# Kernel optimization log

Hardware: AMD Instinct MI355X
Metric: run time of the kernel (lower is better)

## Reference

```python
import jax, jax.numpy as jnp
import numpy as np

LN_EPS = 1e-5
L2_EPS = 1e-12  # torch F.normalize eps


def _layernorm(h, g, b):
    mu = jnp.mean(h, axis=-1, keepdims=True)
    var = jnp.var(h, axis=-1, keepdims=True)
    return (h - mu) * jax.lax.rsqrt(var + LN_EPS) * g + b


def _l2norm(h):
    n = jnp.linalg.norm(h, axis=-1, keepdims=True)
    return h / jnp.maximum(n, L2_EPS)


def _temperature(epoch, total_epochs):
    warmup = total_epochs * 0.1
    if epoch < warmup:
        return 2.0
    progress = (epoch - warmup) / (total_epochs - warmup)
    return max(0.7, 2.0 - 1.3 * progress)


def setup_inputs() -> dict:
    key = jax.random.key(0)
    ks = jax.random.split(key, 4)
    B, T, D, P, C = 8, 4096, 1024, 512, 64
    x = jax.random.normal(ks[0], (B, T, D), dtype=jnp.float32)
    w1 = jax.random.normal(ks[1], (D, C), dtype=jnp.float32) * 0.02
    b1 = jnp.zeros((C,), jnp.float32)
    ln1_g = jnp.ones((C,), jnp.float32)
    ln1_b = jnp.zeros((C,), jnp.float32)
    patterns = jax.random.normal(ks[2], (P, C), dtype=jnp.float32)
    patterns = _l2norm(patterns)  # init is row-orthonormalized in torch via SVD; unit rows suffice
    w2 = jax.random.normal(ks[3], (C, D), dtype=jnp.float32) * 0.02
    b2 = jnp.zeros((D,), jnp.float32)
    ln2_g = jnp.ones((D,), jnp.float32)
    ln2_b = jnp.zeros((D,), jnp.float32)
    return {"x": x, "w1": w1, "b1": b1, "ln1_g": ln1_g, "ln1_b": ln1_b,
            "patterns": patterns, "w2": w2, "b2": b2, "ln2_g": ln2_g, "ln2_b": ln2_b,
            "epoch": 0, "total_epochs": 100}


def reference(x, w1, b1, ln1_g, ln1_b, patterns, w2, b2, ln2_g, ln2_b, epoch, total_epochs):
    n_patterns = patterns.shape[0]
    # bottleneck projection + LayerNorm: [B,T,D] -> [B,T,C]
    Q = _layernorm(jnp.einsum('btd,dc->btc', x, w1) + b1, ln1_g, ln1_b)
    Q_norm = _l2norm(Q)
    K_norm = _l2norm(patterns)  # [P,C]
    temp = _temperature(epoch, total_epochs)
    logits = jnp.einsum('btc,pc->btp', Q_norm, K_norm) / temp  # [B,T,P]
    hard_indices = jnp.argmax(logits, axis=-1)  # [B,T]
    assignments = jax.nn.one_hot(hard_indices, n_patterns, dtype=jnp.float32)  # eval: hard
    pattern_emb_low = jnp.einsum('btp,pc->btc', assignments, patterns)
    pattern_emb = _layernorm(jnp.einsum('btc,cd->btd', pattern_emb_low, w2) + b2, ln2_g, ln2_b)
    return (pattern_emb, assignments, logits, hard_indices, Q)
```

## Files before the change

### kernel.cpp

```cpp
#include <hip/hip_runtime.h>

#define O_PE 0
#define O_AS 33554432
#define O_LG 50331648
#define O_HI 67108864
#define O_Q  67141632

typedef float vf4 __attribute__((ext_vector_type(4)));

__device__ __forceinline__ void nts4(float* p, float4 v) {
  vf4 t; t.x = v.x; t.y = v.y; t.z = v.z; t.w = v.w;
  __builtin_nontemporal_store(t, (vf4*)p);
}
__device__ __forceinline__ float4 ntl4(const float* p) {
  vf4 t = __builtin_nontemporal_load((const vf4*)p);
  float4 r; r.x = t.x; r.y = t.y; r.z = t.z; r.w = t.w;
  return r;
}

__global__ void k0_pre(const float* __restrict__ patterns, const float* __restrict__ w2,
                       const float* __restrict__ b2, const float* __restrict__ ln2g,
                       const float* __restrict__ ln2b, const int* __restrict__ epoch,
                       const int* __restrict__ total_epochs,
                       float* __restrict__ invt, float* __restrict__ knT,
                       float* __restrict__ peb) {
  const int b = blockIdx.x, t = threadIdx.x;
  __shared__ float pat[64];
  __shared__ float red[8];

  if (b == 0 && t == 0) {
    float ep = (float)epoch[0], te = (float)total_epochs[0];
    float warm = te * 0.1f;
    float temp;
    if (ep < warm) temp = 2.0f;
    else {
      float prog = (ep - warm) / (te - warm);
      temp = fmaxf(0.7f, 2.0f - 1.3f * prog);
    }
    invt[0] = 1.0f / temp;
  }

  if (t < 64) pat[t] = patterns[b * 64 + t];
  __syncthreads();

  if (t < 64) {
    float v = pat[t];
    float s = v * v;
    #pragma unroll
    for (int m = 1; m < 64; m <<= 1) s += __shfl_xor(s, m);
    float scale = 1.0f / fmaxf(sqrtf(s), 1e-12f);
    knT[(size_t)t * 512 + b] = v * scale;
  }

  const int d0 = t * 4;
  float4 acc = *(const float4*)&b2[d0];
  #pragma unroll 8
  for (int k = 0; k < 64; ++k) {
    float pk = pat[k];
    float4 w = *(const float4*)&w2[(size_t)k * 1024 + d0];
    acc.x = fmaf(pk, w.x, acc.x);
    acc.y = fmaf(pk, w.y, acc.y);
    acc.z = fmaf(pk, w.z, acc.z);
    acc.w = fmaf(pk, w.w, acc.w);
  }
  float s1 = acc.x + acc.y + acc.z + acc.w;
  float s2 = acc.x*acc.x + acc.y*acc.y + acc.z*acc.z + acc.w*acc.w;
  #pragma unroll
  for (int m = 1; m < 64; m <<= 1) { s1 += __shfl_xor(s1, m); s2 += __shfl_xor(s2, m); }
  const int wid = t >> 6;
  if ((t & 63) == 0) { red[wid] = s1; red[wid + 4] = s2; }
  __syncthreads();
  s1 = red[0] + red[1] + red[2] + red[3];
  s2 = red[4] + red[5] + red[6] + red[7];
  float mu = s1 * (1.0f / 1024.0f);
  float var = s2 * (1.0f / 1024.0f) - mu * mu;
  float rstd = rsqrtf(var + 1e-5f);
  float4 g  = *(const float4*)&ln2g[d0];
  float4 bb = *(const float4*)&ln2b[d0];
  float4 o;
  o.x = (acc.x - mu) * rstd * g.x + bb.x;
  o.y = (acc.y - mu) * rstd * g.y + bb.y;
  o.z = (acc.z - mu) * rstd * g.z + bb.z;
  o.w = (acc.w - mu) * rstd * g.w + bb.w;
  *(float4*)&peb[(size_t)b * 1024 + d0] = o;
}

__global__ __launch_bounds__(256, 2) void k_fused(
    const float* __restrict__ x, const float* __restrict__ w1,
    const float* __restrict__ b1, const float* __restrict__ ln1g,
    const float* __restrict__ ln1b, const float* __restrict__ knT,
    const float* __restrict__ invtp, const float* __restrict__ peb,
    float* __restrict__ outPe, float* __restrict__ outAs,
    float* __restrict__ outLg, float* __restrict__ outHi,
    float* __restrict__ outQ) {
  __shared__ float smem[17408];
  const int tid = threadIdx.x;
  const int rowbase = blockIdx.x * 64;

  const int g  = tid >> 6;
  const int t  = tid & 63;
  const int rt = t >> 3, ct = t & 7;
  const int r0 = rt * 8, c0 = ct * 8;
  const int kbase = g * 256;

  float* xsT = smem;
  float* w1s = smem + 8704;

  float acc[8][8];
  #pragma unroll
  for (int i = 0; i < 8; ++i)
    #pragma unroll
    for (int j = 0; j < 8; ++j) acc[i][j] = 0.f;

  const float* xp = x + (size_t)(rowbase + (t >> 3)) * 1024 + kbase + (t & 7) * 4;
  const int wkr = t >> 4;
  const int wc4 = (t & 15) * 4;

  for (int kt = 0; kt < 8; ++kt) {
    const int kb = kt * 32;
    float4 xv[8], wv[8];
    #pragma unroll
    for (int p = 0; p < 8; ++p)
      xv[p] = ntl4(xp + (size_t)p * 8192 + kb);
    const float* wp = w1 + (size_t)(kbase + kb + wkr) * 64 + wc4;
    #pragma unroll
    for (int p = 0; p < 8; ++p)
      wv[p] = *(const float4*)(wp + (size_t)p * 256);
    __syncthreads();
    {
      const int kc4 = (t & 7) * 4;
      const int sw = 8 * ((kc4 >> 3) & 3);
      #pragma unroll
      for (int p = 0; p < 8; ++p) {
        const int row = ((t >> 3) + 8 * p) ^ sw;
        xsT[g*2176 + (kc4+0)*68 + row] = xv[p].x;
        xsT[g*2176 + (kc4+1)*68 + row] = xv[p].y;
        xsT[g*2176 + (kc4+2)*68 + row] = xv[p].z;
        xsT[g*2176 + (kc4+3)*68 + row] = xv[p].w;
      }
    }
    #pragma unroll
    for (int p = 0; p < 8; ++p)
      *(float4*)&w1s[g*2176 + (wkr + 4*p)*68 + wc4] = wv[p];
    __syncthreads();
    #pragma unroll 4
    for (int kk = 0; kk < 32; ++kk) {
      const int rb = r0 ^ (8 * ((kk >> 3) & 3));
      float4 a0 = *(float4*)&xsT[g*2176 + kk*68 + rb];
      float4 a1 = *(float4*)&xsT[g*2176 + kk*68 + rb + 4];
      float4 b0 = *(float4*)&w1s[g*2176 + kk*68 + c0];
      float4 b1v = *(float4*)&w1s[g*2176 + kk*68 + c0 + 4];
      float av[8] = {a0.x, a0.y, a0.z, a0.w, a1.x, a1.y, a1.z, a1.w};
      float bv[8] = {b0.x, b0.y, b0.z, b0.w, b1v.x, b1v.y, b1v.z, b1v.w};
      #pragma unroll
      for (int i = 0; i < 8; ++i)
        #pragma unroll
        for (int j = 0; j < 8; ++j)
          acc[i][j] = fmaf(av[i], bv[j], acc[i][j]);
    }
  }

  __syncthreads();
  if (g > 0) {
    float* hc = smem + (g - 1) * 4096;
    #pragma unroll
    for (int i = 0; i < 8; ++i) {
      float4 v0, v1;
      v0.x = acc[i][0]; v0.y = acc[i][1]; v0.z = acc[i][2]; v0.w = acc[i][3];
      v1.x = acc[i][4]; v1.y = acc[i][5]; v1.z = acc[i][6]; v1.w = acc[i][7];
      *(float4*)&hc[(r0+i)*64 + c0]     = v0;
      *(float4*)&hc[(r0+i)*64 + c0 + 4] = v1;
    }
  }
  __syncthreads();
  float* qns = smem + 12288;
  if (g == 0) {
    float bb[8], gg[8], ee[8];
    {
      float4 t0 = *(const float4*)&b1[c0];
      float4 t1 = *(const float4*)&b1[c0 + 4];
      float4 t2 = *(const float4*)&ln1g[c0];
      float4 t3 = *(const float4*)&ln1g[c0 + 4];
      float4 t4 = *(const float4*)&ln1b[c0];
      float4 t5 = *(const float4*)&ln1b[c0 + 4];
      bb[0]=t0.x; bb[1]=t0.y; bb[2]=t0.z; bb[3]=t0.w; bb[4]=t1.x; bb[5]=t1.y; bb[6]=t1.z; bb[7]=t1.w;
      gg[0]=t2.x; gg[1]=t2.y; gg[2]=t2.z; gg[3]=t2.w; gg[4]=t3.x; gg[5]=t3.y; gg[6]=t3.z; gg[7]=t3.w;
      ee[0]=t4.x; ee[1]=t4.y; ee[2]=t4.z; ee[3]=t4.w; ee[4]=t5.x; ee[5]=t5.y; ee[6]=t5.z; ee[7]=t5.w;
    }
    #pragma unroll
    for (int i = 0; i < 8; ++i) {
      const int row = r0 + i;
      float h[8];
      #pragma unroll
      for (int j = 0; j < 8; ++j) h[j] = acc[i][j] + bb[j];
      #pragma unroll
      for (int gg2 = 0; gg2 < 3; ++gg2) {
        float4 p0 = *(float4*)&smem[gg2*4096 + row*64 + c0];
        float4 p1 = *(float4*)&smem[gg2*4096 + row*64 + c0 + 4];
        h[0] += p0.x; h[1] += p0.y; h[2] += p0.z; h[3] += p0.w;
        h[4] += p1.x; h[5] += p1.y; h[6] += p1.z; h[7] += p1.w;
      }
      float s1 = 0.f, s2 = 0.f;
      #pragma unroll
      for (int j = 0; j < 8; ++j) { s1 += h[j]; s2 += h[j]*h[j]; }
      #pragma unroll
      for (int m = 1; m < 8; m <<= 1) { s1 += __shfl_xor(s1, m); s2 += __shfl_xor(s2, m); }
      const float mu   = s1 * 0.015625f;
      const float var  = s2 * 0.015625f - mu * mu;
      const float rstd = rsqrtf(var + 1e-5f);
      float q[8]; float t2s = 0.f;
      #pragma unroll
      for (int j = 0; j < 8; ++j) { q[j] = (h[j] - mu) * rstd * gg[j] + ee[j]; t2s += q[j]*q[j]; }
      #pragma unroll
      for (int m = 1; m < 8; m <<= 1) t2s += __shfl_xor(t2s, m);
      const float scl = 1.0f / fmaxf(sqrtf(t2s), 1e-12f);
      float4 qa, qc;
      qa.x = q[0]; qa.y = q[1]; qa.z = q[2]; qa.w = q[3];
      qc.x = q[4]; qc.y = q[5]; qc.z = q[6]; qc.w = q[7];
      nts4(&outQ[(size_t)(rowbase + row) * 64 + c0], qa);
      nts4(&outQ[(size_t)(rowbase + row) * 64 + c0 + 4], qc);
      #pragma unroll
      for (int j = 0; j < 8; ++j) qns[row*68 + c0 + j] = q[j] * scl;
    }
  }
  __syncthreads();

  const float invt = invtp[0];
  const int lane = tid & 63;
  const int w    = tid >> 6;
  const int brt  = lane & 3;
  const int pt16 = lane >> 2;
  const int pbase = w * 128 + pt16 * 8;

  float* avm = smem;
  int*   avi = (int*)(smem + 256);
  int*   sidx = (int*)(smem + 512);

  float a2[16][8];
  #pragma unroll
  for (int i = 0; i < 16; ++i)
    #pragma unroll
    for (int j = 0; j < 8; ++j) a2[i][j] = 0.f;

  for (int cb = 0; cb < 16; ++cb) {
    float kv[4][8];
    #pragma unroll
    for (int dc = 0; dc < 4; ++dc) {
      float4 k0 = *(const float4*)&knT[(size_t)(cb*4+dc)*512 + pbase];
      float4 k1 = *(const float4*)&knT[(size_t)(cb*4+dc)*512 + pbase + 4];
      kv[dc][0]=k0.x; kv[dc][1]=k0.y; kv[dc][2]=k0.z; kv[dc][3]=k0.w;
      kv[dc][4]=k1.x; kv[dc][5]=k1.y; kv[dc][6]=k1.z; kv[dc][7]=k1.w;
    }
    #pragma unroll
    for (int i = 0; i < 16; ++i) {
      float4 qv = *(float4*)&qns[(brt + 4*i)*68 + cb*4];
      float qq[4] = {qv.x, qv.y, qv.z, qv.w};
      #pragma unroll
      for (int dc = 0; dc < 4; ++dc)
        #pragma unroll
        for (int j = 0; j < 8; ++j)
          a2[i][j] = fmaf(qq[dc], kv[dc][j], a2[i][j]);
    }
  }

  #pragma unroll
  for (int i = 0; i < 16; ++i) {
    const int row = brt + 4*i;
    const size_t grow = (size_t)(rowbase + row);
    float v[8];
    float bm = -3.0e38f; int bi = 0;
    #pragma unroll
    for (int j = 0; j < 8; ++j) {
      v[j] = a2[i][j] * invt;
      if (v[j] > bm) { bm = v[j]; bi = pbase + j; }
    }
    float4 o0, o1;
    o0.x = v[0]; o0.y = v[1]; o0.z = v[2]; o0.w = v[3];
    o1.x = v[4]; o1.y = v[5]; o1.z = v[6]; o1.w = v[7];
    nts4(&outLg[grow * 512 + pbase], o0);
    nts4(&outLg[grow * 512 + pbase + 4], o1);
    #pragma unroll
    for (int m = 4; m < 64; m <<= 1) {
      float ov = __shfl_xor(bm, m);
      int   oi = __shfl_xor(bi, m);
      if (ov > bm || (ov == bm && oi < bi)) { bm = ov; bi = oi; }
    }
    if (pt16 == 0) { avm[w*64 + row] = bm; avi[w*64 + row] = bi; }
  }
  __syncthreads();

  if (tid < 64) {
    float bm = avm[tid]; int bi = avi[tid];
    #pragma unroll
    for (int w2 = 1; w2 < 4; ++w2) {
      float m = avm[w2*64 + tid];
      int   i = avi[w2*64 + tid];
      if (m > bm) { bm = m; bi = i; }
    }
    sidx[tid] = bi;
    __builtin_nontemporal_store((float)bi, &outHi[rowbase + tid]);
  }
  __syncthreads();

  #pragma unroll
  for (int p = 0; p < 32; ++p) {
    const int id = tid + p * 256;
    const int r = id >> 7, c4 = (id & 127) * 4;
    const int b = sidx[r];
    float4 z; z.x = 0.f; z.y = 0.f; z.z = 0.f; z.w = 0.f;
    if (b >= c4 && b < c4 + 4) ((float*)&z)[b - c4] = 1.0f;
    nts4(&outAs[(size_t)(rowbase + r) * 512 + c4], z);
  }

  #pragma unroll 4
  for (int p = 0; p < 64; ++p) {
    const int id = tid + p * 256;
    const int r = id >> 8, c4 = id & 255;
    float4 pv = *(const float4*)&peb[((size_t)sidx[r] * 256 + c4) * 4];
    nts4(&outPe[((size_t)(rowbase + r) * 256 + c4) * 4], pv);
  }
}

extern "C" void kernel_launch(void* const* d_in, const int* in_sizes, int n_in,
                              void* d_out, int out_size, void* d_ws, size_t ws_size,
                              hipStream_t stream) {
  (void)in_sizes; (void)n_in; (void)out_size; (void)ws_size;
  const float* x        = (const float*)d_in[0];
  const float* w1       = (const float*)d_in[1];
  const float* b1       = (const float*)d_in[2];
  const float* ln1g     = (const float*)d_in[3];
  const float* ln1b     = (const float*)d_in[4];
  const float* patterns = (const float*)d_in[5];
  const float* w2       = (const float*)d_in[6];
  const float* b2       = (const float*)d_in[7];
  const float* ln2g     = (const float*)d_in[8];
  const float* ln2b     = (const float*)d_in[9];
  const int*   epoch    = (const int*)d_in[10];
  const int*   total    = (const int*)d_in[11];

  float* out = (float*)d_out;
  float* outPe = out + O_PE;
  float* outAs = out + O_AS;
  float* outLg = out + O_LG;
  float* outHi = out + O_HI;
  float* outQ  = out + O_Q;

  float* wsf  = (float*)d_ws;
  float* invt = wsf;
  float* knT  = wsf + 64;
  float* peb  = (float*)((char*)d_ws + 131328);

  hipLaunchKernelGGL(k0_pre, dim3(512), dim3(256), 0, stream,
                     patterns, w2, b2, ln2g, ln2b, epoch, total, invt, knT, peb);
  hipLaunchKernelGGL(k_fused, dim3(512), dim3(256), 0, stream,
                     x, w1, b1, ln1g, ln1b, knT, invt, peb,
                     outPe, outAs, outLg, outHi, outQ);
}
```

Baseline: 156.2 us.

## Double block size to 512 threads with 8-way split-K and tree reduction

Launches the fused kernel with 512 threads per block instead of 256. The first GEMM's K dimension is now split across 8 wavefront groups of 128 instead of 4 of 256, and partial sums are combined with a shared-memory tree reduction. The logits stage and the output writes are also redistributed so each thread handles half as many rows. The aim is more waves in flight for latency hiding on this memory-bound kernel, at the cost of extra barriers and reduction steps and possibly tighter register limits from the launch bounds.

```diff
diff --git a/kernel.cpp b/kernel.cpp
--- a/kernel.cpp
+++ b/kernel.cpp
@@ -85,7 +85,7 @@
   *(float4*)&peb[(size_t)b * 1024 + d0] = o;
 }
 
-__global__ __launch_bounds__(256, 2) void k_fused(
+__global__ __launch_bounds__(512, 4) void k_fused(
     const float* __restrict__ x, const float* __restrict__ w1,
     const float* __restrict__ b1, const float* __restrict__ ln1g,
     const float* __restrict__ ln1b, const float* __restrict__ knT,
@@ -101,10 +101,10 @@
   const int t  = tid & 63;
   const int rt = t >> 3, ct = t & 7;
   const int r0 = rt * 8, c0 = ct * 8;
-  const int kbase = g * 256;
-
-  float* xsT = smem;
-  float* w1s = smem + 8704;
+  const int kbase = g * 128;
+
+  float* xsT = smem + g * 1088;
+  float* w1s = smem + 8704 + g * 1088;
 
   float acc[8][8];
   #pragma unroll
@@ -112,44 +112,43 @@
     #pragma unroll
     for (int j = 0; j < 8; ++j) acc[i][j] = 0.f;
 
-  const float* xp = x + (size_t)(rowbase + (t >> 3)) * 1024 + kbase + (t & 7) * 4;
+  const int srow = t >> 2;
+  const int skc4 = (t & 3) * 4;
+  const int ssw  = 8 * ((skc4 >> 3) & 1);
+  const float* xp = x + (size_t)(rowbase + srow) * 1024 + kbase + skc4;
   const int wkr = t >> 4;
   const int wc4 = (t & 15) * 4;
+  const float* wp0 = w1 + (size_t)(kbase + wkr) * 64 + wc4;
 
   for (int kt = 0; kt < 8; ++kt) {
-    const int kb = kt * 32;
-    float4 xv[8], wv[8];
-    #pragma unroll
-    for (int p = 0; p < 8; ++p)
-      xv[p] = ntl4(xp + (size_t)p * 8192 + kb);
-    const float* wp = w1 + (size_t)(kbase + kb + wkr) * 64 + wc4;
-    #pragma unroll
-    for (int p = 0; p < 8; ++p)
-      wv[p] = *(const float4*)(wp + (size_t)p * 256);
+    const int kb = kt * 16;
+    float4 xv[4], wv[4];
+    #pragma unroll
+    for (int p = 0; p < 4; ++p)
+      xv[p] = ntl4(xp + (size_t)p * 16384 + kb);
+    #pragma unroll
+    for (int p = 0; p < 4; ++p)
+      wv[p] = *(const float4*)(wp0 + (size_t)(kb + 4 * p) * 64);
     __syncthreads();
-    {
-      const int kc4 = (t & 7) * 4;
-      const int sw = 8 * ((kc4 >> 3) & 3);
-      #pragma unroll
-      for (int p = 0; p < 8; ++p) {
-        const int row = ((t >> 3) + 8 * p) ^ sw;
-        xsT[g*2176 + (kc4+0)*68 + row] = xv[p].x;
-        xsT[g*2176 + (kc4+1)*68 + row] = xv[p].y;
-        xsT[g*2176 + (kc4+2)*68 + row] = xv[p].z;
-        xsT[g*2176 + (kc4+3)*68 + row] = xv[p].w;
-      }
-    }
-    #pragma unroll
-    for (int p = 0; p < 8; ++p)
-      *(float4*)&w1s[g*2176 + (wkr + 4*p)*68 + wc4] = wv[p];
+    #pragma unroll
+    for (int p = 0; p < 4; ++p) {
+      const int row = (srow + 16 * p) ^ ssw;
+      xsT[(skc4+0)*68 + row] = xv[p].x;
+      xsT[(skc4+1)*68 + row] = xv[p].y;
+      xsT[(skc4+2)*68 + row] = xv[p].z;
+      xsT[(skc4+3)*68 + row] = xv[p].w;
+    }
+    #pragma unroll
+    for (int p = 0; p < 4; ++p)
+      *(float4*)&w1s[(wkr + 4*p)*68 + wc4] = wv[p];
     __syncthreads();
     #pragma unroll 4
-    for (int kk = 0; kk < 32; ++kk) {
-      const int rb = r0 ^ (8 * ((kk >> 3) & 3));
-      float4 a0 = *(float4*)&xsT[g*2176 + kk*68 + rb];
-      float4 a1 = *(float4*)&xsT[g*2176 + kk*68 + rb + 4];
-      float4 b0 = *(float4*)&w1s[g*2176 + kk*68 + c0];
-      float4 b1v = *(float4*)&w1s[g*2176 + kk*68 + c0 + 4];
+    for (int kk = 0; kk < 16; ++kk) {
+      const int rb = r0 ^ (8 * ((kk >> 3) & 1));
+      float4 a0 = *(float4*)&xsT[kk*68 + rb];
+      float4 a1 = *(float4*)&xsT[kk*68 + rb + 4];
+      float4 b0 = *(float4*)&w1s[kk*68 + c0];
+      float4 b1v = *(float4*)&w1s[kk*68 + c0 + 4];
       float av[8] = {a0.x, a0.y, a0.z, a0.w, a1.x, a1.y, a1.z, a1.w};
       float bv[8] = {b0.x, b0.y, b0.z, b0.w, b1v.x, b1v.y, b1v.z, b1v.w};
       #pragma unroll
@@ -161,8 +160,8 @@
   }
 
   __syncthreads();
-  if (g > 0) {
-    float* hc = smem + (g - 1) * 4096;
+  if (g & 1) {
+    float* hc = smem + (g >> 1) * 4096;
     #pragma unroll
     for (int i = 0; i < 8; ++i) {
       float4 v0, v1;
@@ -173,7 +172,53 @@
     }
   }
   __syncthreads();
-  float* qns = smem + 12288;
+  if (!(g & 1)) {
+    float* hc = smem + (g >> 1) * 4096;
+    #pragma unroll
+    for (int i = 0; i < 8; ++i) {
+      float4 p0 = *(float4*)&hc[(r0+i)*64 + c0];
+      float4 p1 = *(float4*)&hc[(r0+i)*64 + c0 + 4];
+      acc[i][0] += p0.x; acc[i][1] += p0.y; acc[i][2] += p0.z; acc[i][3] += p0.w;
+      acc[i][4] += p1.x; acc[i][5] += p1.y; acc[i][6] += p1.z; acc[i][7] += p1.w;
+    }
+  }
+  __syncthreads();
+  if (g == 2 || g == 6) {
+    float* hc = smem + ((g - 2) >> 2) * 4096;
+    #pragma unroll
+    for (int i = 0; i < 8; ++i) {
+      float4 v0, v1;
+      v0.x = acc[i][0]; v0.y = acc[i][1]; v0.z = acc[i][2]; v0.w = acc[i][3];
+      v1.x = acc[i][4]; v1.y = acc[i][5]; v1.z = acc[i][6]; v1.w = acc[i][7];
+      *(float4*)&hc[(r0+i)*64 + c0]     = v0;
+      *(float4*)&hc[(r0+i)*64 + c0 + 4] = v1;
+    }
+  }
+  __syncthreads();
+  if (g == 0 || g == 4) {
+    float* hc = smem + (g >> 2) * 4096;
+    #pragma unroll
+    for (int i = 0; i < 8; ++i) {
+      float4 p0 = *(float4*)&hc[(r0+i)*64 + c0];
+      float4 p1 = *(float4*)&hc[(r0+i)*64 + c0 + 4];
+      acc[i][0] += p0.x; acc[i][1] += p0.y; acc[i][2] += p0.z; acc[i][3] += p0.w;
+      acc[i][4] += p1.x; acc[i][5] += p1.y; acc[i][6] += p1.z; acc[i][7] += p1.w;
+    }
+  }
+  __syncthreads();
+  if (g == 4) {
+    #pragma unroll
+    for (int i = 0; i < 8; ++i) {
+      float4 v0, v1;
+      v0.x = acc[i][0]; v0.y = acc[i][1]; v0.z = acc[i][2]; v0.w = acc[i][3];
+      v1.x = acc[i][4]; v1.y = acc[i][5]; v1.z = acc[i][6]; v1.w = acc[i][7];
+      *(float4*)&smem[(r0+i)*64 + c0]     = v0;
+      *(float4*)&smem[(r0+i)*64 + c0 + 4] = v1;
+    }
+  }
+  __syncthreads();
+
+  float* qns = smem + 8704;
   if (g == 0) {
     float bb[8], gg[8], ee[8];
     {
@@ -193,13 +238,10 @@
       float h[8];
       #pragma unroll
       for (int j = 0; j < 8; ++j) h[j] = acc[i][j] + bb[j];
-      #pragma unroll
-      for (int gg2 = 0; gg2 < 3; ++gg2) {
-        float4 p0 = *(float4*)&smem[gg2*4096 + row*64 + c0];
-        float4 p1 = *(float4*)&smem[gg2*4096 + row*64 + c0 + 4];
-        h[0] += p0.x; h[1] += p0.y; h[2] += p0.z; h[3] += p0.w;
-        h[4] += p1.x; h[5] += p1.y; h[6] += p1.z; h[7] += p1.w;
-      }
+      float4 p0 = *(float4*)&smem[row*64 + c0];
+      float4 p1 = *(float4*)&smem[row*64 + c0 + 4];
+      h[0] += p0.x; h[1] += p0.y; h[2] += p0.z; h[3] += p0.w;
+      h[4] += p1.x; h[5] += p1.y; h[6] += p1.z; h[7] += p1.w;
       float s1 = 0.f, s2 = 0.f;
       #pragma unroll
       for (int j = 0; j < 8; ++j) { s1 += h[j]; s2 += h[j]*h[j]; }
@@ -227,18 +269,18 @@
 
   const float invt = invtp[0];
   const int lane = tid & 63;
-  const int w    = tid >> 6;
-  const int brt  = lane & 3;
-  const int pt16 = lane >> 2;
-  const int pbase = w * 128 + pt16 * 8;
-
-  float* avm = smem;
-  int*   avi = (int*)(smem + 256);
-  int*   sidx = (int*)(smem + 512);
-
-  float a2[16][8];
+  const int w8   = tid >> 6;
+  const int pt8  = lane >> 3;
+  const int brt  = lane & 7;
+  const int pbase = w8 * 64 + pt8 * 8;
+
+  float* avm = smem + 13056;
+  int*   avi = (int*)(smem + 13568);
+  int*   sidx = (int*)(smem + 14080);
+
+  float a2[8][8];
   #pragma unroll
-  for (int i = 0; i < 16; ++i)
+  for (int i = 0; i < 8; ++i)
     #pragma unroll
     for (int j = 0; j < 8; ++j) a2[i][j] = 0.f;
 
@@ -252,8 +294,8 @@
       kv[dc][4]=k1.x; kv[dc][5]=k1.y; kv[dc][6]=k1.z; kv[dc][7]=k1.w;
     }
     #pragma unroll
-    for (int i = 0; i < 16; ++i) {
-      float4 qv = *(float4*)&qns[(brt + 4*i)*68 + cb*4];
+    for (int i = 0; i < 8; ++i) {
+      float4 qv = *(float4*)&qns[(brt + 8*i)*68 + cb*4];
       float qq[4] = {qv.x, qv.y, qv.z, qv.w};
       #pragma unroll
       for (int dc = 0; dc < 4; ++dc)
@@ -264,8 +306,8 @@
   }
 
   #pragma unroll
-  for (int i = 0; i < 16; ++i) {
-    const int row = brt + 4*i;
+  for (int i = 0; i < 8; ++i) {
+    const int row = brt + 8*i;
     const size_t grow = (size_t)(rowbase + row);
     float v[8];
     float bm = -3.0e38f; int bi = 0;
@@ -280,19 +322,19 @@
     nts4(&outLg[grow * 512 + pbase], o0);
     nts4(&outLg[grow * 512 + pbase + 4], o1);
     #pragma unroll
-    for (int m = 4; m < 64; m <<= 1) {
+    for (int m = 8; m < 64; m <<= 1) {
       float ov = __shfl_xor(bm, m);
       int   oi = __shfl_xor(bi, m);
       if (ov > bm || (ov == bm && oi < bi)) { bm = ov; bi = oi; }
     }
-    if (pt16 == 0) { avm[w*64 + row] = bm; avi[w*64 + row] = bi; }
+    if (pt8 == 0) { avm[w8*64 + row] = bm; avi[w8*64 + row] = bi; }
   }
   __syncthreads();
 
   if (tid < 64) {
     float bm = avm[tid]; int bi = avi[tid];
     #pragma unroll
-    for (int w2 = 1; w2 < 4; ++w2) {
+    for (int w2 = 1; w2 < 8; ++w2) {
       float m = avm[w2*64 + tid];
       int   i = avi[w2*64 + tid];
       if (m > bm) { bm = m; bi = i; }
@@ -303,8 +345,8 @@
   __syncthreads();
 
   #pragma unroll
-  for (int p = 0; p < 32; ++p) {
-    const int id = tid + p * 256;
+  for (int p = 0; p < 16; ++p) {
+    const int id = tid + p * 512;
     const int r = id >> 7, c4 = (id & 127) * 4;
     const int b = sidx[r];
     float4 z; z.x = 0.f; z.y = 0.f; z.z = 0.f; z.w = 0.f;
@@ -313,8 +355,8 @@
   }
 
   #pragma unroll 4
-  for (int p = 0; p < 64; ++p) {
-    const int id = tid + p * 256;
+  for (int p = 0; p < 32; ++p) {
+    const int id = tid + p * 512;
     const int r = id >> 8, c4 = id & 255;
     float4 pv = *(const float4*)&peb[((size_t)sidx[r] * 256 + c4) * 4];
     nts4(&outPe[((size_t)(rowbase + r) * 256 + c4) * 4], pv);
@@ -352,7 +394,7 @@
 
   hipLaunchKernelGGL(k0_pre, dim3(512), dim3(256), 0, stream,
                      patterns, w2, b2, ln2g, ln2b, epoch, total, invt, knT, peb);
-  hipLaunchKernelGGL(k_fused, dim3(512), dim3(256), 0, stream,
+  hipLaunchKernelGGL(k_fused, dim3(512), dim3(512), 0, stream,
                      x, w1, b1, ln1g, ln1b, knT, invt, peb,
                      outPe, outAs, outLg, outHi, outQ);
 }
```

Result: slower. 169.5 us (+8.5%).

## Halve rows per block and drop LDS staging for the projection GEMM

Applied to the files above, without the earlier changes.

Each block now handles 32 rows instead of 64, doubling the grid to 1024 blocks. The x·w1 projection reads x and w1 straight from global memory into registers instead of staging transposed tiles in shared memory, which removes per-tile barriers and cuts LDS use. The split-K partial sums are reduced as a tree in shared memory. The aim is more resident blocks and better latency hiding on this memory-bound kernel, at the cost of redundant w1 reads through cache and less reuse per thread.

```diff
diff --git a/kernel.cpp b/kernel.cpp
--- a/kernel.cpp
+++ b/kernel.cpp
@@ -93,113 +93,113 @@
     float* __restrict__ outPe, float* __restrict__ outAs,
     float* __restrict__ outLg, float* __restrict__ outHi,
     float* __restrict__ outQ) {
-  __shared__ float smem[17408];
+  __shared__ float smem[6560];
   const int tid = threadIdx.x;
-  const int rowbase = blockIdx.x * 64;
+  const int rowbase = blockIdx.x * 32;
 
   const int g  = tid >> 6;
   const int t  = tid & 63;
   const int rt = t >> 3, ct = t & 7;
-  const int r0 = rt * 8, c0 = ct * 8;
   const int kbase = g * 256;
 
-  float* xsT = smem;
-  float* w1s = smem + 8704;
-
-  float acc[8][8];
-  #pragma unroll
-  for (int i = 0; i < 8; ++i)
+  float acc[4][8];
+  #pragma unroll
+  for (int i = 0; i < 4; ++i)
     #pragma unroll
     for (int j = 0; j < 8; ++j) acc[i][j] = 0.f;
 
-  const float* xp = x + (size_t)(rowbase + (t >> 3)) * 1024 + kbase + (t & 7) * 4;
-  const int wkr = t >> 4;
-  const int wc4 = (t & 15) * 4;
-
-  for (int kt = 0; kt < 8; ++kt) {
-    const int kb = kt * 32;
-    float4 xv[8], wv[8];
-    #pragma unroll
-    for (int p = 0; p < 8; ++p)
-      xv[p] = ntl4(xp + (size_t)p * 8192 + kb);
-    const float* wp = w1 + (size_t)(kbase + kb + wkr) * 64 + wc4;
-    #pragma unroll
-    for (int p = 0; p < 8; ++p)
-      wv[p] = *(const float4*)(wp + (size_t)p * 256);
-    __syncthreads();
-    {
-      const int kc4 = (t & 7) * 4;
-      const int sw = 8 * ((kc4 >> 3) & 3);
-      #pragma unroll
-      for (int p = 0; p < 8; ++p) {
-        const int row = ((t >> 3) + 8 * p) ^ sw;
-        xsT[g*2176 + (kc4+0)*68 + row] = xv[p].x;
-        xsT[g*2176 + (kc4+1)*68 + row] = xv[p].y;
-        xsT[g*2176 + (kc4+2)*68 + row] = xv[p].z;
-        xsT[g*2176 + (kc4+3)*68 + row] = xv[p].w;
-      }
-    }
-    #pragma unroll
-    for (int p = 0; p < 8; ++p)
-      *(float4*)&w1s[g*2176 + (wkr + 4*p)*68 + wc4] = wv[p];
-    __syncthreads();
-    #pragma unroll 4
-    for (int kk = 0; kk < 32; ++kk) {
-      const int rb = r0 ^ (8 * ((kk >> 3) & 3));
-      float4 a0 = *(float4*)&xsT[g*2176 + kk*68 + rb];
-      float4 a1 = *(float4*)&xsT[g*2176 + kk*68 + rb + 4];
-      float4 b0 = *(float4*)&w1s[g*2176 + kk*68 + c0];
-      float4 b1v = *(float4*)&w1s[g*2176 + kk*68 + c0 + 4];
-      float av[8] = {a0.x, a0.y, a0.z, a0.w, a1.x, a1.y, a1.z, a1.w};
-      float bv[8] = {b0.x, b0.y, b0.z, b0.w, b1v.x, b1v.y, b1v.z, b1v.w};
-      #pragma unroll
-      for (int i = 0; i < 8; ++i)
-        #pragma unroll
-        for (int j = 0; j < 8; ++j)
-          acc[i][j] = fmaf(av[i], bv[j], acc[i][j]);
-    }
-  }
-
-  __syncthreads();
-  if (g > 0) {
-    float* hc = smem + (g - 1) * 4096;
-    #pragma unroll
-    for (int i = 0; i < 8; ++i) {
+  const float* xa = x + (size_t)(rowbase + rt) * 1024 + kbase;
+  const float* wb = w1 + (size_t)kbase * 64 + ct * 8;
+
+  #pragma unroll 2
+  for (int kk4 = 0; kk4 < 64; ++kk4) {
+    float4 av[4];
+    #pragma unroll
+    for (int i = 0; i < 4; ++i)
+      av[i] = ntl4(xa + (size_t)8192 * i + 4 * kk4);
+    const float* wk = wb + (size_t)(4 * kk4) * 64;
+#define ASTEP(DC, COMP)                                                     \
+    {                                                                       \
+      float4 b0 = *(const float4*)(wk + (size_t)DC * 64);                   \
+      float4 b1v = *(const float4*)(wk + (size_t)DC * 64 + 4);              \
+      _Pragma("unroll")                                                     \
+      for (int i = 0; i < 4; ++i) {                                         \
+        const float ai = av[i].COMP;                                        \
+        acc[i][0] = fmaf(ai, b0.x, acc[i][0]);                              \
+        acc[i][1] = fmaf(ai, b0.y, acc[i][1]);                              \
+        acc[i][2] = fmaf(ai, b0.z, acc[i][2]);                              \
+        acc[i][3] = fmaf(ai, b0.w, acc[i][3]);                              \
+        acc[i][4] = fmaf(ai, b1v.x, acc[i][4]);                             \
+        acc[i][5] = fmaf(ai, b1v.y, acc[i][5]);                             \
+        acc[i][6] = fmaf(ai, b1v.z, acc[i][6]);                             \
+        acc[i][7] = fmaf(ai, b1v.w, acc[i][7]);                             \
+      }                                                                     \
+    }
+    ASTEP(0, x) ASTEP(1, y) ASTEP(2, z) ASTEP(3, w)
+#undef ASTEP
+  }
+
+  float* hacc0 = smem;
+  float* hacc1 = smem + 2048;
+  float* qns   = smem + 4096;
+
+  if (g == 1 || g == 3) {
+    float* hc = (g == 1) ? hacc0 : hacc1;
+    #pragma unroll
+    for (int i = 0; i < 4; ++i) {
       float4 v0, v1;
       v0.x = acc[i][0]; v0.y = acc[i][1]; v0.z = acc[i][2]; v0.w = acc[i][3];
       v1.x = acc[i][4]; v1.y = acc[i][5]; v1.z = acc[i][6]; v1.w = acc[i][7];
-      *(float4*)&hc[(r0+i)*64 + c0]     = v0;
-      *(float4*)&hc[(r0+i)*64 + c0 + 4] = v1;
-    }
-  }
-  __syncthreads();
-  float* qns = smem + 12288;
+      *(float4*)&hc[(rt + 8*i)*64 + ct*8]     = v0;
+      *(float4*)&hc[(rt + 8*i)*64 + ct*8 + 4] = v1;
+    }
+  }
+  __syncthreads();
+  if (g == 0 || g == 2) {
+    float* hc = (g == 0) ? hacc0 : hacc1;
+    #pragma unroll
+    for (int i = 0; i < 4; ++i) {
+      float4 p0 = *(float4*)&hc[(rt + 8*i)*64 + ct*8];
+      float4 p1 = *(float4*)&hc[(rt + 8*i)*64 + ct*8 + 4];
+      acc[i][0] += p0.x; acc[i][1] += p0.y; acc[i][2] += p0.z; acc[i][3] += p0.w;
+      acc[i][4] += p1.x; acc[i][5] += p1.y; acc[i][6] += p1.z; acc[i][7] += p1.w;
+    }
+  }
+  __syncthreads();
+  if (g == 2) {
+    #pragma unroll
+    for (int i = 0; i < 4; ++i) {
+      float4 v0, v1;
+      v0.x = acc[i][0]; v0.y = acc[i][1]; v0.z = acc[i][2]; v0.w = acc[i][3];
+      v1.x = acc[i][4]; v1.y = acc[i][5]; v1.z = acc[i][6]; v1.w = acc[i][7];
+      *(float4*)&hacc0[(rt + 8*i)*64 + ct*8]     = v0;
+      *(float4*)&hacc0[(rt + 8*i)*64 + ct*8 + 4] = v1;
+    }
+  }
+  __syncthreads();
   if (g == 0) {
     float bb[8], gg[8], ee[8];
     {
-      float4 t0 = *(const float4*)&b1[c0];
-      float4 t1 = *(const float4*)&b1[c0 + 4];
-      float4 t2 = *(const float4*)&ln1g[c0];
-      float4 t3 = *(const float4*)&ln1g[c0 + 4];
-      float4 t4 = *(const float4*)&ln1b[c0];
-      float4 t5 = *(const float4*)&ln1b[c0 + 4];
+      float4 t0 = *(const float4*)&b1[ct*8];
+      float4 t1 = *(const float4*)&b1[ct*8 + 4];
+      float4 t2 = *(const float4*)&ln1g[ct*8];
+      float4 t3 = *(const float4*)&ln1g[ct*8 + 4];
+      float4 t4 = *(const float4*)&ln1b[ct*8];
+      float4 t5 = *(const float4*)&ln1b[ct*8 + 4];
       bb[0]=t0.x; bb[1]=t0.y; bb[2]=t0.z; bb[3]=t0.w; bb[4]=t1.x; bb[5]=t1.y; bb[6]=t1.z; bb[7]=t1.w;
       gg[0]=t2.x; gg[1]=t2.y; gg[2]=t2.z; gg[3]=t2.w; gg[4]=t3.x; gg[5]=t3.y; gg[6]=t3.z; gg[7]=t3.w;
       ee[0]=t4.x; ee[1]=t4.y; ee[2]=t4.z; ee[3]=t4.w; ee[4]=t5.x; ee[5]=t5.y; ee[6]=t5.z; ee[7]=t5.w;
     }
     #pragma unroll
-    for (int i = 0; i < 8; ++i) {
-      const int row = r0 + i;
+    for (int i = 0; i < 4; ++i) {
+      const int row = rt + 8*i;
       float h[8];
-      #pragma unroll
-      for (int j = 0; j < 8; ++j) h[j] = acc[i][j] + bb[j];
-      #pragma unroll
-      for (int gg2 = 0; gg2 < 3; ++gg2) {
-        float4 p0 = *(float4*)&smem[gg2*4096 + row*64 + c0];
-        float4 p1 = *(float4*)&smem[gg2*4096 + row*64 + c0 + 4];
-        h[0] += p0.x; h[1] += p0.y; h[2] += p0.z; h[3] += p0.w;
-        h[4] += p1.x; h[5] += p1.y; h[6] += p1.z; h[7] += p1.w;
-      }
+      float4 p0 = *(float4*)&hacc0[row*64 + ct*8];
+      float4 p1 = *(float4*)&hacc0[row*64 + ct*8 + 4];
+      h[0] = acc[i][0] + p0.x + bb[0]; h[1] = acc[i][1] + p0.y + bb[1];
+      h[2] = acc[i][2] + p0.z + bb[2]; h[3] = acc[i][3] + p0.w + bb[3];
+      h[4] = acc[i][4] + p1.x + bb[4]; h[5] = acc[i][5] + p1.y + bb[5];
+      h[6] = acc[i][6] + p1.z + bb[6]; h[7] = acc[i][7] + p1.w + bb[7];
       float s1 = 0.f, s2 = 0.f;
       #pragma unroll
       for (int j = 0; j < 8; ++j) { s1 += h[j]; s2 += h[j]*h[j]; }
@@ -217,10 +217,10 @@
       float4 qa, qc;
       qa.x = q[0]; qa.y = q[1]; qa.z = q[2]; qa.w = q[3];
       qc.x = q[4]; qc.y = q[5]; qc.z = q[6]; qc.w = q[7];
-      nts4(&outQ[(size_t)(rowbase + row) * 64 + c0], qa);
-      nts4(&outQ[(size_t)(rowbase + row) * 64 + c0 + 4], qc);
-      #pragma unroll
-      for (int j = 0; j < 8; ++j) qns[row*68 + c0 + j] = q[j] * scl;
+      nts4(&outQ[(size_t)(rowbase + row) * 64 + ct*8], qa);
+      nts4(&outQ[(size_t)(rowbase + row) * 64 + ct*8 + 4], qc);
+      #pragma unroll
+      for (int j = 0; j < 8; ++j) qns[row*68 + ct*8 + j] = q[j] * scl;
     }
   }
   __syncthreads();
@@ -232,13 +232,13 @@
   const int pt16 = lane >> 2;
   const int pbase = w * 128 + pt16 * 8;
 
-  float* avm = smem;
-  int*   avi = (int*)(smem + 256);
-  int*   sidx = (int*)(smem + 512);
-
-  float a2[16][8];
-  #pragma unroll
-  for (int i = 0; i < 16; ++i)
+  float* avm = smem + 6272;
+  int*   avi = (int*)(smem + 6400);
+  int*   sidx = (int*)(smem + 6528);
+
+  float a2[8][8];
+  #pragma unroll
+  for (int i = 0; i < 8; ++i)
     #pragma unroll
     for (int j = 0; j < 8; ++j) a2[i][j] = 0.f;
 
@@ -252,7 +252,7 @@
       kv[dc][4]=k1.x; kv[dc][5]=k1.y; kv[dc][6]=k1.z; kv[dc][7]=k1.w;
     }
     #pragma unroll
-    for (int i = 0; i < 16; ++i) {
+    for (int i = 0; i < 8; ++i) {
       float4 qv = *(float4*)&qns[(brt + 4*i)*68 + cb*4];
       float qq[4] = {qv.x, qv.y, qv.z, qv.w};
       #pragma unroll
@@ -264,7 +264,7 @@
   }
 
   #pragma unroll
-  for (int i = 0; i < 16; ++i) {
+  for (int i = 0; i < 8; ++i) {
     const int row = brt + 4*i;
     const size_t grow = (size_t)(rowbase + row);
     float v[8];
@@ -285,16 +285,16 @@
       int   oi = __shfl_xor(bi, m);
       if (ov > bm || (ov == bm && oi < bi)) { bm = ov; bi = oi; }
     }
-    if (pt16 == 0) { avm[w*64 + row] = bm; avi[w*64 + row] = bi; }
-  }
-  __syncthreads();
-
-  if (tid < 64) {
+    if (pt16 == 0) { avm[w*32 + row] = bm; avi[w*32 + row] = bi; }
+  }
+  __syncthreads();
+
+  if (tid < 32) {
     float bm = avm[tid]; int bi = avi[tid];
     #pragma unroll
     for (int w2 = 1; w2 < 4; ++w2) {
-      float m = avm[w2*64 + tid];
-      int   i = avi[w2*64 + tid];
+      float m = avm[w2*32 + tid];
+      int   i = avi[w2*32 + tid];
       if (m > bm) { bm = m; bi = i; }
     }
     sidx[tid] = bi;
@@ -303,7 +303,7 @@
   __syncthreads();
 
   #pragma unroll
-  for (int p = 0; p < 32; ++p) {
+  for (int p = 0; p < 16; ++p) {
     const int id = tid + p * 256;
     const int r = id >> 7, c4 = (id & 127) * 4;
     const int b = sidx[r];
@@ -313,7 +313,7 @@
   }
 
   #pragma unroll 4
-  for (int p = 0; p < 64; ++p) {
+  for (int p = 0; p < 32; ++p) {
     const int id = tid + p * 256;
     const int r = id >> 8, c4 = id & 255;
     float4 pv = *(const float4*)&peb[((size_t)sidx[r] * 256 + c4) * 4];
@@ -352,7 +352,7 @@
 
   hipLaunchKernelGGL(k0_pre, dim3(512), dim3(256), 0, stream,
                      patterns, w2, b2, ln2g, ln2b, epoch, total, invt, knT, peb);
-  hipLaunchKernelGGL(k_fused, dim3(512), dim3(256), 0, stream,
+  hipLaunchKernelGGL(k_fused, dim3(1024), dim3(256), 0, stream,
                      x, w1, b1, ln1g, ln1b, knT, invt, peb,
                      outPe, outAs, outLg, outHi, outQ);
 }
```

Measured after the change: 233.1 us. 1.49x slower.
